# Performance work log

Hardware: AMD Instinct MI355X
Metric: run time of the kernel (lower is better)

Reference implementation:

```python
import jax, jax.numpy as jnp
import numpy as np

H = 512
B = 64
T = 256


def setup_inputs() -> dict:
    key = jax.random.key(0)
    k1, k2, k3 = jax.random.split(key, 3)
    seq_type_embed = jax.random.normal(k1, (B, T, H), dtype=jnp.float32)
    dtime = jax.random.uniform(k2, (B, T), dtype=jnp.float32)
    # 7 fused Dense layers: concat([x_t, h_t]) (width 2H) -> 7H outputs
    scale = 1.0 / np.sqrt(2.0 * H)
    W = jax.random.normal(k3, (2 * H, 7 * H), dtype=jnp.float32) * scale
    b = jnp.zeros((7 * H,), dtype=jnp.float32)
    return {"seq_type_embed": seq_type_embed, "dtime": dtime, "W": W, "b": b}


def _cell(W, b, x_t, dt, h, c_func, c_bar):
    # x_t: [B,H], dt: [B], h/c_func/c_bar: [B,H]
    inp = jnp.concatenate([x_t, h], axis=-1)          # [B, 2H]
    g = inp @ W + b                                   # [B, 7H] fused gate GEMM
    gi, gf, go, gib, gfb, gd, gz = jnp.split(g, 7, axis=-1)
    gate_input = jax.nn.sigmoid(gi)
    gate_forget = jax.nn.sigmoid(gf)
    gate_output = jax.nn.sigmoid(go)
    gate_input_bar = jax.nn.sigmoid(gib)
    gate_forget_bar = jax.nn.sigmoid(gfb)
    gate_decay = jax.nn.softplus(gd)
    z_t = jnp.tanh(gz)
    c_t = gate_forget * c_func + gate_input * z_t
    c_bar_t = gate_forget_bar * c_bar + gate_input_bar * z_t
    # Equation (7): exponential decay toward c_bar
    c_func_t = c_bar_t + (c_t - c_bar_t) * jnp.exp(-gate_decay * dt[:, None])
    h_t = gate_output * jnp.tanh(c_func_t)
    return h_t, c_func_t, c_bar_t, c_t, gate_decay, gate_output


def reference(seq_type_embed, dtime, W, b):
    Bb, Tt, Hh = seq_type_embed.shape

    def step(carry, xs):
        h, c_func, c_bar = carry
        x_t, dt = xs
        h_t, c_func_t, c_bar_t, c_t, gate_decay, gate_output = _cell(
            W, b, x_t, dt, h, c_func, c_bar)
        decay_t = jnp.stack([c_t, c_bar_t, gate_decay, gate_output], axis=1)  # [B,4,H]
        return (h_t, c_func_t, c_bar_t), (h_t, decay_t)

    z = jnp.zeros((Bb, Hh), dtype=seq_type_embed.dtype)
    init = (z, z, z)
    xs = (jnp.swapaxes(seq_type_embed, 0, 1), jnp.swapaxes(dtime, 0, 1))  # time-major
    _, (h_ts, decay_ts) = jax.lax.scan(step, init, xs)
    h_ts = jnp.swapaxes(h_ts, 0, 1)            # [B, T, H]
    decay_states = jnp.swapaxes(decay_ts, 0, 1)  # [B, T, 4, H]
    return h_ts, decay_states
```

## Files before the change

### kernel.cpp

```cpp
#include <hip/hip_runtime.h>
#include <hip/hip_bf16.h>

#define Hh  512
#define Bb  64
#define Tt  256
#define G7  3584
#define NWG 128

typedef __attribute__((ext_vector_type(8))) short short8;
typedef __attribute__((ext_vector_type(4))) float f32x4;

union U16 { unsigned long long q[2]; short8 v; };

static __device__ __forceinline__ unsigned short f2bf(float f) {
  unsigned int u = __float_as_uint(f);
  unsigned int lsb = (u >> 16) & 1u;
  u += 0x7fffu + lsb;
  return (unsigned short)(u >> 16);
}

static __device__ __forceinline__ float sigmoidf_(float x) {
  return 1.0f / (1.0f + expf(-x));
}
static __device__ __forceinline__ float softplusf_(float x) {
  return fmaxf(x, 0.0f) + log1pf(expf(-fabsf(x)));
}

__global__ void k_pack_w(const float* __restrict__ W, unsigned short* __restrict__ wp) {
  int t = blockIdx.x * 256 + threadIdx.x;
  int l  = t & 63;
  int nf = (t >> 6) & 1;
  int kf = (t >> 7) & 31;
  int wg = t >> 12;
  int pcol  = nf * 16 + (l & 15);
  int kbase = kf * 32 + (l >> 4) * 8;
  unsigned int o[4];
  if (pcol < 28) {
    int g = pcol >> 2, r = pcol & 3;
    int col = g * 512 + wg * 4 + r;
    const float* src = W + (size_t)kbase * G7 + col;
#pragma unroll
    for (int j = 0; j < 4; ++j) {
      unsigned short a = f2bf(src[(size_t)(2 * j) * G7]);
      unsigned short b = f2bf(src[(size_t)(2 * j + 1) * G7]);
      o[j] = (unsigned int)a | ((unsigned int)b << 16);
    }
  } else {
    o[0] = o[1] = o[2] = o[3] = 0u;
  }
  unsigned long long* q = (unsigned long long*)(wp + (size_t)t * 8);
  q[0] = (unsigned long long)o[0] | ((unsigned long long)o[1] << 32);
  q[1] = (unsigned long long)o[2] | ((unsigned long long)o[3] << 32);
}

__global__ void k_xt(const float* __restrict__ X, unsigned short* __restrict__ xT) {
  int t = blockIdx.x * 256 + threadIdx.x;
  int k4 = t & 127;
  int b  = (t >> 7) & 63;
  int tt = t >> 13;
  const float4* in = (const float4*)(X + ((size_t)(b * Tt + tt) * Hh + k4 * 4));
  float4 f = *in;
  unsigned int p0 = (unsigned)f2bf(f.x) | ((unsigned)f2bf(f.y) << 16);
  unsigned int p1 = (unsigned)f2bf(f.z) | ((unsigned)f2bf(f.w) << 16);
  unsigned long long v = (unsigned long long)p0 | ((unsigned long long)p1 << 32);
  *(unsigned long long*)(xT + ((size_t)(tt * Bb + b) * Hh + k4 * 4)) = v;
}

__global__ void k_init(unsigned int* __restrict__ z, int n) {
  for (int i = blockIdx.x * 256 + threadIdx.x; i < n; i += gridDim.x * 256) z[i] = 0u;
}

__global__ __launch_bounds__(256, 1) void k_seq(
    const unsigned short* __restrict__ wp,
    const unsigned short* __restrict__ xT,
    const float* __restrict__ bias,
    const float* __restrict__ dtime,
    unsigned short* __restrict__ hbuf,
    unsigned int* __restrict__ flags,
    float* __restrict__ out) {

  const int wg   = blockIdx.x;
  const int tid  = threadIdx.x;
  const int wave = tid >> 6;
  const int lane = tid & 63;

  __shared__ float g_lds[64 * 33];
  __shared__ unsigned cnt;
  if (tid == 0) cnt = 0u;

  short8 w[32][2];
  {
    const short8* base = reinterpret_cast<const short8*>(wp);
#pragma unroll
    for (int kf = 0; kf < 32; ++kf) {
#pragma unroll
      for (int nf = 0; nf < 2; ++nf) {
        w[kf][nf] = base[((size_t)(wg * 32 + kf) * 2 + nf) * 64 + lane];
        asm volatile("" : "+v"(w[kf][nf]));
      }
    }
  }

  const int eb   = tid >> 2;
  const int er   = tid & 3;
  const int jcol = wg * 4 + er;
  float bs[7];
#pragma unroll
  for (int g = 0; g < 7; ++g) bs[g] = bias[g * 512 + jcol];

  const int aoff = (wave * 16 + (lane & 15)) * 512 + (lane >> 4) * 8;

  float cf = 0.0f, cb = 0.0f;

  __syncthreads();

  for (int t = 0; t < Tt; ++t) {
    f32x4 acc00 = {0.f, 0.f, 0.f, 0.f};
    f32x4 acc01 = {0.f, 0.f, 0.f, 0.f};
    f32x4 acc10 = {0.f, 0.f, 0.f, 0.f};
    f32x4 acc11 = {0.f, 0.f, 0.f, 0.f};

    float dt = dtime[eb * Tt + t];

    const unsigned short* xp = xT + (size_t)t * (Bb * Hh) + aoff;
#pragma unroll
    for (int kf = 0; kf < 16; ++kf) {
      short8 a = *reinterpret_cast<const short8*>(xp + kf * 32);
      if (kf & 1) {
        acc01 = __builtin_amdgcn_mfma_f32_16x16x32_bf16(a, w[kf][0], acc01, 0, 0, 0);
        acc11 = __builtin_amdgcn_mfma_f32_16x16x32_bf16(a, w[kf][1], acc11, 0, 0, 0);
      } else {
        acc00 = __builtin_amdgcn_mfma_f32_16x16x32_bf16(a, w[kf][0], acc00, 0, 0, 0);
        acc10 = __builtin_amdgcn_mfma_f32_16x16x32_bf16(a, w[kf][1], acc10, 0, 0, 0);
      }
    }

    if (t > 0) {
      unsigned tgt = (unsigned)t;
      int guard = 0;
      for (;;) {
        unsigned a = __hip_atomic_load(flags + lane,      __ATOMIC_RELAXED, __HIP_MEMORY_SCOPE_AGENT);
        unsigned b = __hip_atomic_load(flags + 64 + lane, __ATOMIC_RELAXED, __HIP_MEMORY_SCOPE_AGENT);
        if (__all(a >= tgt && b >= tgt)) break;
        if (++guard > (1 << 16)) break;
      }
      __builtin_amdgcn_sched_barrier(0);
    }

    const unsigned long long* hp8 = reinterpret_cast<const unsigned long long*>(
        hbuf + (size_t)((t & 1) ^ 1) * (Bb * Hh)) + (aoff >> 2);
    short8 hf[16];
#pragma unroll
    for (int kf = 0; kf < 16; ++kf) {
      U16 u;
      u.q[0] = __hip_atomic_load(hp8 + kf * 8,     __ATOMIC_RELAXED, __HIP_MEMORY_SCOPE_AGENT);
      u.q[1] = __hip_atomic_load(hp8 + kf * 8 + 1, __ATOMIC_RELAXED, __HIP_MEMORY_SCOPE_AGENT);
      hf[kf] = u.v;
    }
#pragma unroll
    for (int kf = 0; kf < 16; ++kf) {
      if (kf & 1) {
        acc01 = __builtin_amdgcn_mfma_f32_16x16x32_bf16(hf[kf], w[16 + kf][0], acc01, 0, 0, 0);
        acc11 = __builtin_amdgcn_mfma_f32_16x16x32_bf16(hf[kf], w[16 + kf][1], acc11, 0, 0, 0);
      } else {
        acc00 = __builtin_amdgcn_mfma_f32_16x16x32_bf16(hf[kf], w[16 + kf][0], acc00, 0, 0, 0);
        acc10 = __builtin_amdgcn_mfma_f32_16x16x32_bf16(hf[kf], w[16 + kf][1], acc10, 0, 0, 0);
      }
    }

    {
      f32x4 s0 = acc00 + acc01;
      f32x4 s1 = acc10 + acc11;
      int colbase = lane & 15;
      int row0 = wave * 16 + (lane >> 4) * 4;
#pragma unroll
      for (int q = 0; q < 4; ++q) g_lds[(row0 + q) * 33 + colbase] = s0[q];
#pragma unroll
      for (int q = 0; q < 4; ++q) g_lds[(row0 + q) * 33 + 16 + colbase] = s1[q];
    }
    __syncthreads();

    float gv[7];
#pragma unroll
    for (int g = 0; g < 7; ++g) gv[g] = g_lds[eb * 33 + g * 4 + er] + bs[g];

    float gi  = sigmoidf_(gv[0]);
    float gf  = sigmoidf_(gv[1]);
    float go  = sigmoidf_(gv[2]);
    float gib = sigmoidf_(gv[3]);
    float gfb = sigmoidf_(gv[4]);
    float gd  = softplusf_(gv[5]);
    float zt  = tanhf(gv[6]);

    float c_t    = gf * cf + gi * zt;
    float cbar_t = gfb * cb + gib * zt;
    float cfn    = cbar_t + (c_t - cbar_t) * expf(-gd * dt);
    float h      = go * tanhf(cfn);
    cf = cfn;
    cb = cbar_t;

    {
      unsigned hb16 = (unsigned)f2bf(h);
      unsigned other = (unsigned)__shfl_xor((int)hb16, 1);
      unsigned pair = hb16 | (other << 16);
      unsigned pair_hi = (unsigned)__shfl_xor((int)pair, 2);
      if (er == 0) {
        unsigned long long v = (unsigned long long)pair |
                               ((unsigned long long)pair_hi << 32);
        unsigned long long* hw = reinterpret_cast<unsigned long long*>(
            hbuf + (size_t)(t & 1) * (Bb * Hh) + eb * Hh + wg * 4);
        __hip_atomic_store(hw, v, __ATOMIC_RELAXED, __HIP_MEMORY_SCOPE_AGENT);
      }
    }

    asm volatile("s_waitcnt vmcnt(0)" ::: "memory");
    if (lane == 0) {
      unsigned old = __hip_atomic_fetch_add(&cnt, 1u, __ATOMIC_RELAXED,
                                            __HIP_MEMORY_SCOPE_WORKGROUP);
      if (old == (unsigned)(4 * t + 3)) {
        __hip_atomic_store(flags + wg, (unsigned)(t + 1),
                           __ATOMIC_RELAXED, __HIP_MEMORY_SCOPE_AGENT);
      }
    }

    size_t ho = (size_t)(eb * Tt + t) * Hh + jcol;
    out[ho] = h;
    size_t db = (size_t)8388608 + (size_t)((eb * Tt + t) * 4) * Hh + jcol;
    out[db]        = c_t;
    out[db + 512]  = cbar_t;
    out[db + 1024] = gd;
    out[db + 1536] = go;
  }
}

extern "C" void kernel_launch(void* const* d_in, const int* in_sizes, int n_in,
                              void* d_out, int out_size, void* d_ws, size_t ws_size,
                              hipStream_t stream) {
  const float* X  = (const float*)d_in[0];
  const float* dt = (const float*)d_in[1];
  const float* W  = (const float*)d_in[2];
  const float* bi = (const float*)d_in[3];
  float* out = (float*)d_out;

  char* ws = (char*)d_ws;
  unsigned short* wp   = (unsigned short*)(ws);
  unsigned short* xT   = (unsigned short*)(ws + 8388608);
  unsigned short* hb   = (unsigned short*)(ws + 25165824);
  unsigned int*  zbase = (unsigned int*)(ws + 25165824);
  unsigned int*  flg   = (unsigned int*)(ws + 25296896);

  k_pack_w<<<2048, 256, 0, stream>>>(W, wp);
  k_xt<<<8192, 256, 0, stream>>>(X, xT);
  k_init<<<64, 256, 0, stream>>>(zbase, 32896);
  k_seq<<<NWG, 256, 0, stream>>>(wp, xT, bi, dt, hb, flg, out);
}
```

Before: 2.500 ms.

## Split gate GEMM across waves by K-slice with x and h on separate waves

Each wave previously handled 16 batch rows across the full K=1024 reduction. Now each wave owns a quarter of K (two waves do the input projection, two do the recurrent h projection) across all 64 rows, and partial sums are reduced through LDS. The x-part waves no longer wait on the inter-workgroup flag, so only half the MFMA work sits behind the h dependency, and each wave holds 8 weight fragments instead of 32, which cuts register pressure. The cost is a larger LDS reduction with an extra barrier per step, plus a longer spin-guard limit.

```diff
diff --git a/kernel.cpp b/kernel.cpp
--- a/kernel.cpp
+++ b/kernel.cpp
@@ -84,18 +84,18 @@
   const int wave = tid >> 6;
   const int lane = tid & 63;
 
-  __shared__ float g_lds[64 * 33];
+  __shared__ float part[4 * 32 * 68];
   __shared__ unsigned cnt;
   if (tid == 0) cnt = 0u;
 
-  short8 w[32][2];
+  short8 w[8][2];
   {
     const short8* base = reinterpret_cast<const short8*>(wp);
 #pragma unroll
-    for (int kf = 0; kf < 32; ++kf) {
+    for (int kf = 0; kf < 8; ++kf) {
 #pragma unroll
       for (int nf = 0; nf < 2; ++nf) {
-        w[kf][nf] = base[((size_t)(wg * 32 + kf) * 2 + nf) * 64 + lane];
+        w[kf][nf] = base[((size_t)(wg * 32 + wave * 8 + kf) * 2 + nf) * 64 + lane];
         asm volatile("" : "+v"(w[kf][nf]));
       }
     }
@@ -108,81 +108,89 @@
 #pragma unroll
   for (int g = 0; g < 7; ++g) bs[g] = bias[g * 512 + jcol];
 
-  const int aoff = (wave * 16 + (lane & 15)) * 512 + (lane >> 4) * 8;
+  const int arow  = lane & 15;
+  const int ak    = (lane >> 4) * 8;
+  const int kbase = (wave & 1) * 256;
+  const bool ish  = wave >= 2;
 
   float cf = 0.0f, cb = 0.0f;
 
   __syncthreads();
 
   for (int t = 0; t < Tt; ++t) {
-    f32x4 acc00 = {0.f, 0.f, 0.f, 0.f};
-    f32x4 acc01 = {0.f, 0.f, 0.f, 0.f};
-    f32x4 acc10 = {0.f, 0.f, 0.f, 0.f};
-    f32x4 acc11 = {0.f, 0.f, 0.f, 0.f};
-
     float dt = dtime[eb * Tt + t];
 
-    const unsigned short* xp = xT + (size_t)t * (Bb * Hh) + aoff;
-#pragma unroll
-    for (int kf = 0; kf < 16; ++kf) {
-      short8 a = *reinterpret_cast<const short8*>(xp + kf * 32);
-      if (kf & 1) {
-        acc01 = __builtin_amdgcn_mfma_f32_16x16x32_bf16(a, w[kf][0], acc01, 0, 0, 0);
-        acc11 = __builtin_amdgcn_mfma_f32_16x16x32_bf16(a, w[kf][1], acc11, 0, 0, 0);
-      } else {
-        acc00 = __builtin_amdgcn_mfma_f32_16x16x32_bf16(a, w[kf][0], acc00, 0, 0, 0);
-        acc10 = __builtin_amdgcn_mfma_f32_16x16x32_bf16(a, w[kf][1], acc10, 0, 0, 0);
-      }
-    }
-
-    if (t > 0) {
-      unsigned tgt = (unsigned)t;
-      int guard = 0;
-      for (;;) {
-        unsigned a = __hip_atomic_load(flags + lane,      __ATOMIC_RELAXED, __HIP_MEMORY_SCOPE_AGENT);
-        unsigned b = __hip_atomic_load(flags + 64 + lane, __ATOMIC_RELAXED, __HIP_MEMORY_SCOPE_AGENT);
-        if (__all(a >= tgt && b >= tgt)) break;
-        if (++guard > (1 << 16)) break;
-      }
-      __builtin_amdgcn_sched_barrier(0);
-    }
-
-    const unsigned long long* hp8 = reinterpret_cast<const unsigned long long*>(
-        hbuf + (size_t)((t & 1) ^ 1) * (Bb * Hh)) + (aoff >> 2);
-    short8 hf[16];
-#pragma unroll
-    for (int kf = 0; kf < 16; ++kf) {
-      U16 u;
-      u.q[0] = __hip_atomic_load(hp8 + kf * 8,     __ATOMIC_RELAXED, __HIP_MEMORY_SCOPE_AGENT);
-      u.q[1] = __hip_atomic_load(hp8 + kf * 8 + 1, __ATOMIC_RELAXED, __HIP_MEMORY_SCOPE_AGENT);
-      hf[kf] = u.v;
-    }
-#pragma unroll
-    for (int kf = 0; kf < 16; ++kf) {
-      if (kf & 1) {
-        acc01 = __builtin_amdgcn_mfma_f32_16x16x32_bf16(hf[kf], w[16 + kf][0], acc01, 0, 0, 0);
-        acc11 = __builtin_amdgcn_mfma_f32_16x16x32_bf16(hf[kf], w[16 + kf][1], acc11, 0, 0, 0);
-      } else {
-        acc00 = __builtin_amdgcn_mfma_f32_16x16x32_bf16(hf[kf], w[16 + kf][0], acc00, 0, 0, 0);
-        acc10 = __builtin_amdgcn_mfma_f32_16x16x32_bf16(hf[kf], w[16 + kf][1], acc10, 0, 0, 0);
-      }
-    }
-
-    {
-      f32x4 s0 = acc00 + acc01;
-      f32x4 s1 = acc10 + acc11;
-      int colbase = lane & 15;
-      int row0 = wave * 16 + (lane >> 4) * 4;
-#pragma unroll
-      for (int q = 0; q < 4; ++q) g_lds[(row0 + q) * 33 + colbase] = s0[q];
-#pragma unroll
-      for (int q = 0; q < 4; ++q) g_lds[(row0 + q) * 33 + 16 + colbase] = s1[q];
-    }
+    f32x4 acc[4][2];
+#pragma unroll
+    for (int m = 0; m < 4; ++m)
+#pragma unroll
+      for (int nf = 0; nf < 2; ++nf) acc[m][nf] = f32x4{0.f, 0.f, 0.f, 0.f};
+
+    if (!ish) {
+      const unsigned short* xp = xT + (size_t)t * (Bb * Hh);
+#pragma unroll
+      for (int kf = 0; kf < 8; ++kf) {
+        short8 a[4];
+#pragma unroll
+        for (int m = 0; m < 4; ++m)
+          a[m] = *reinterpret_cast<const short8*>(
+              xp + (m * 16 + arow) * Hh + kbase + kf * 32 + ak);
+#pragma unroll
+        for (int m = 0; m < 4; ++m) {
+          acc[m][0] = __builtin_amdgcn_mfma_f32_16x16x32_bf16(a[m], w[kf][0], acc[m][0], 0, 0, 0);
+          acc[m][1] = __builtin_amdgcn_mfma_f32_16x16x32_bf16(a[m], w[kf][1], acc[m][1], 0, 0, 0);
+        }
+      }
+    } else {
+      if (t > 0) {
+        unsigned tgt = (unsigned)t;
+        int guard = 0;
+        for (;;) {
+          unsigned a = __hip_atomic_load(flags + lane,      __ATOMIC_RELAXED, __HIP_MEMORY_SCOPE_AGENT);
+          unsigned b = __hip_atomic_load(flags + 64 + lane, __ATOMIC_RELAXED, __HIP_MEMORY_SCOPE_AGENT);
+          if (__all(a >= tgt && b >= tgt)) break;
+          if (++guard > (1 << 17)) break;
+        }
+        __builtin_amdgcn_sched_barrier(0);
+      }
+      const unsigned long long* hp = reinterpret_cast<const unsigned long long*>(
+          hbuf + (size_t)((t & 1) ^ 1) * (Bb * Hh));
+#pragma unroll
+      for (int kf = 0; kf < 8; ++kf) {
+        short8 a[4];
+#pragma unroll
+        for (int m = 0; m < 4; ++m) {
+          U16 u;
+          int eo = (m * 16 + arow) * Hh + kbase + kf * 32 + ak;
+          u.q[0] = __hip_atomic_load(hp + (eo >> 2),     __ATOMIC_RELAXED, __HIP_MEMORY_SCOPE_AGENT);
+          u.q[1] = __hip_atomic_load(hp + (eo >> 2) + 1, __ATOMIC_RELAXED, __HIP_MEMORY_SCOPE_AGENT);
+          a[m] = u.v;
+        }
+#pragma unroll
+        for (int m = 0; m < 4; ++m) {
+          acc[m][0] = __builtin_amdgcn_mfma_f32_16x16x32_bf16(a[m], w[kf][0], acc[m][0], 0, 0, 0);
+          acc[m][1] = __builtin_amdgcn_mfma_f32_16x16x32_bf16(a[m], w[kf][1], acc[m][1], 0, 0, 0);
+        }
+      }
+    }
+
+#pragma unroll
+    for (int m = 0; m < 4; ++m)
+#pragma unroll
+      for (int nf = 0; nf < 2; ++nf) {
+        int wd = wave * 2176 + (nf * 16 + arow) * 68 + m * 16 + (lane >> 4) * 4;
+        *reinterpret_cast<f32x4*>(&part[wd]) = acc[m][nf];
+      }
     __syncthreads();
 
     float gv[7];
 #pragma unroll
-    for (int g = 0; g < 7; ++g) gv[g] = g_lds[eb * 33 + g * 4 + er] + bs[g];
+    for (int g = 0; g < 7; ++g) {
+      int n = g * 4 + er;
+      gv[g] = part[0 * 2176 + n * 68 + eb] + part[1 * 2176 + n * 68 + eb] +
+              part[2 * 2176 + n * 68 + eb] + part[3 * 2176 + n * 68 + eb] + bs[g];
+    }
+    __syncthreads();
 
     float gi  = sigmoidf_(gv[0]);
     float gf  = sigmoidf_(gv[1]);
```

Result: slower. 3.252 ms (+30.1%).
